# Performance work log

Hardware: AMD Instinct MI355X
Metric: run time of the kernel (lower is better)

The kernel has to match this reference:

```python
import jax, jax.numpy as jnp
import numpy as np

N_NODES = 50000
NODE_DIM = 128
HIDDEN = 128
N_EDGES = 1600000
N_POSTS = 8192


def setup_inputs() -> dict:
    key = jax.random.key(0)
    ks = jax.random.split(key, 12)
    glorot = lambda k, shp: jax.random.normal(k, shp, jnp.float32) * (1.0 / np.sqrt(shp[0]))
    inp = {
        "node_features": jax.random.normal(ks[0], (N_NODES, NODE_DIM), jnp.float32),
        "edge_index": jax.random.randint(ks[1], (2, N_EDGES), 0, N_NODES, jnp.int32),
        "post_mask": jax.random.randint(ks[2], (N_POSTS,), 0, N_NODES, jnp.int32),
        # node_encoder: node_dim -> hidden
        "W_enc": glorot(ks[3], (NODE_DIM, HIDDEN)),
        "b_enc": jnp.zeros((HIDDEN,), jnp.float32),
        # conv1/conv2: hidden -> hidden
        "W1": glorot(ks[4], (HIDDEN, HIDDEN)),
        "b1": jnp.zeros((HIDDEN,), jnp.float32),
        "W2": glorot(ks[5], (HIDDEN, HIDDEN)),
        "b2": jnp.zeros((HIDDEN,), jnp.float32),
        # output head: hidden -> hidden//2 -> 1
        "W_o1": glorot(ks[6], (HIDDEN, HIDDEN // 2)),
        "b_o1": jnp.zeros((HIDDEN // 2,), jnp.float32),
        "W_o2": glorot(ks[7], (HIDDEN // 2, 1)),
        "b_o2": jnp.zeros((1,), jnp.float32),
    }
    return inp


def _aggregate(h, src, dst, n_nodes):
    # sum_{e: dst[e]=v} h[src[e]]  -- vectorized scatter-add (segment_sum)
    return jax.ops.segment_sum(h[src], dst, num_segments=n_nodes)


def reference(node_features, edge_index, post_mask,
              W_enc, b_enc, W1, b1, W2, b2, W_o1, b_o1, W_o2, b_o2):
    src, dst = edge_index[0], edge_index[1]
    n = node_features.shape[0]

    h = jax.nn.relu(node_features @ W_enc + b_enc)          # [N, H]
    agg = _aggregate(h, src, dst, n)                        # [N, H]
    h = jax.nn.relu((agg + h) @ W1 + b1)
    agg = _aggregate(h, src, dst, n)
    h = jax.nn.relu((agg + h) @ W2 + b2)

    post = h[post_mask]                                     # [P, H]
    hid = jax.nn.relu(post @ W_o1 + b_o1)                   # [P, H//2]
    logits = (hid @ W_o2 + b_o2).squeeze(-1)                # [P]
    return jax.nn.sigmoid(logits)
```

## Files before the change

### kernel.cpp

```cpp
#include <hip/hip_runtime.h>
#include <math.h>


typedef unsigned long long u64;

#define RB_SIZE    4096
#define RB_ROUNDS  16
#define BUCKET_CAP 9216

__global__ __launch_bounds__(1024) void scan_part(const int* __restrict__ in,
                                                  int* __restrict__ bsum, int n) {
    __shared__ int red[1024];
    int i = blockIdx.x * 1024 + threadIdx.x;
    red[threadIdx.x] = (i < n) ? in[i] : 0;
    __syncthreads();
    for (int d = 512; d; d >>= 1) {
        if (threadIdx.x < d) red[threadIdx.x] += red[threadIdx.x + d];
        __syncthreads();
    }
    if (threadIdx.x == 0) bsum[blockIdx.x] = red[0];
}

__global__ __launch_bounds__(256) void scan_tops_par(const int* __restrict__ bsum,
                                                     int* __restrict__ bbase, int nb) {
    __shared__ int buf[256];
    int tid = threadIdx.x;
    int v = (tid < nb) ? bsum[tid] : 0;
    buf[tid] = v;
    __syncthreads();
    for (int s = 1; s < 256; s <<= 1) {
        int u = (tid >= s) ? buf[tid - s] : 0;
        __syncthreads();
        buf[tid] += u;
        __syncthreads();
    }
    if (tid < nb) bbase[tid] = buf[tid] - v;
}

__global__ __launch_bounds__(1024) void scan_final(const int* __restrict__ in,
                                                   const int* __restrict__ bbase,
                                                   int* __restrict__ out, int n) {
    __shared__ int buf[1024];
    int tid = threadIdx.x;
    int i = blockIdx.x * 1024 + tid;
    int c = (i < n) ? in[i] : 0;
    buf[tid] = c;
    __syncthreads();
    for (int d = 1; d < 1024; d <<= 1) {
        int v = (tid >= d) ? buf[tid - d] : 0;
        __syncthreads();
        buf[tid] += v;
        __syncthreads();
    }
    if (i < n) out[i] = bbase[blockIdx.x] + buf[tid] - c;
}

__global__ __launch_bounds__(256) void radix_hist_hi(const int* __restrict__ dstArr,
                                                     int* __restrict__ blockhist,
                                                     int E, int NBLK) {
    __shared__ int cnt[256];
    cnt[threadIdx.x] = 0;
    __syncthreads();
    int base = blockIdx.x * RB_SIZE;
    for (int t = threadIdx.x; t < RB_SIZE; t += 256) {
        int i = base + t;
        if (i < E) atomicAdd(&cnt[dstArr[i] >> 8], 1);
    }
    __syncthreads();
    blockhist[threadIdx.x * NBLK + blockIdx.x] = cnt[threadIdx.x];
}

__global__ __launch_bounds__(256) void radix_scatter_hi(const int* __restrict__ dstArr,
                                                        const int* __restrict__ srcArr,
                                                        u64* __restrict__ recOut,
                                                        const int* __restrict__ blockbase,
                                                        int E, int NBLK) {
    __shared__ int cursor[256];
    __shared__ int gbase[256];
    __shared__ int cnt[256 * 4];
    __shared__ int wbase[256 * 4];
    int tid = threadIdx.x;
    int wid = tid >> 6, lane = tid & 63;
    cursor[tid] = 0;
    gbase[tid] = blockbase[tid * NBLK + blockIdx.x];
    int base = blockIdx.x * RB_SIZE;
    __syncthreads();
    for (int r = 0; r < RB_ROUNDS; ++r) {
        int i = base + r * 256 + tid;
        bool valid = (i < E);
        int d = 0;
        u64 rec = 0;
        if (valid) {
            int dv = dstArr[i];
            rec = ((u64)(unsigned)srcArr[i] << 32) | (unsigned)dv;
            d = dv >> 8;
        }
        ((int4*)cnt)[tid] = make_int4(0, 0, 0, 0);
        u64 mask = ~0ull;
#pragma unroll
        for (int b = 0; b < 8; ++b) {
            int bit = (d >> b) & 1;
            u64 bal = __ballot(bit);
            mask &= bit ? bal : ~bal;
        }
        mask &= __ballot(valid ? 1 : 0);
        int rank = __popcll(mask & (((u64)1 << lane) - 1));
        int wtot = __popcll(mask);
        __syncthreads();
        if (valid && rank == 0) cnt[d * 4 + wid] = wtot;
        __syncthreads();
        {
            int run = cursor[tid];
#pragma unroll
            for (int w = 0; w < 4; ++w) {
                wbase[tid * 4 + w] = run;
                run += cnt[tid * 4 + w];
            }
            cursor[tid] = run;
        }
        __syncthreads();
        if (valid) recOut[gbase[d] + wbase[d * 4 + wid] + rank] = rec;
        __syncthreads();
    }
}

__global__ __launch_bounds__(256) void bucket_kernel(const u64* __restrict__ rec,
                                                     const int* __restrict__ blockbase,
                                                     int* __restrict__ csr_src,
                                                     int* __restrict__ offs,
                                                     int E, int N, int NBLK, int NDIG) {
    __shared__ int srcs[BUCKET_CAP];
    __shared__ unsigned char lob[BUCKET_CAP];
    __shared__ int binb[256];
    __shared__ int cursor[256];
    __shared__ int cnt4[256 * 4];
    __shared__ int wbase4[256 * 4];
    int g = blockIdx.x;
    int tid = threadIdx.x;
    int wid = tid >> 6, lane = tid & 63;
    int gbeg = blockbase[g * NBLK];
    int gend = (g + 1 < NDIG) ? blockbase[(g + 1) * NBLK] : E;
    int cnt = gend - gbeg;
    if (cnt > BUCKET_CAP) cnt = BUCKET_CAP;
    binb[tid] = 0;
    __syncthreads();
    for (int i = tid; i < cnt; i += 256) {
        u64 r = rec[gbeg + i];
        srcs[i] = (int)(r >> 32);
        int lo = (int)(r & 255);
        lob[i] = (unsigned char)lo;
        atomicAdd(&binb[lo], 1);
    }
    __syncthreads();
    int c = binb[tid];
    cursor[tid] = c;
    __syncthreads();
    for (int s = 1; s < 256; s <<= 1) {
        int v = (tid >= s) ? cursor[tid - s] : 0;
        __syncthreads();
        cursor[tid] += v;
        __syncthreads();
    }
    int excl = cursor[tid] - c;
    __syncthreads();
    binb[tid] = excl;
    cursor[tid] = excl;
    int v = g * 256 + tid;
    if (v < N) offs[v] = gbeg + excl;
    if (g == NDIG - 1 && tid == 0) offs[N] = E;
    __syncthreads();
    int nrounds = (cnt + 255) >> 8;
    for (int r = 0; r < nrounds; ++r) {
        int i = r * 256 + tid;
        bool valid = (i < cnt);
        int d = valid ? (int)lob[i] : 0;
        ((int4*)cnt4)[tid] = make_int4(0, 0, 0, 0);
        u64 mask = ~0ull;
#pragma unroll
        for (int b = 0; b < 8; ++b) {
            int bit = (d >> b) & 1;
            u64 bal = __ballot(bit);
            mask &= bit ? bal : ~bal;
        }
        mask &= __ballot(valid ? 1 : 0);
        int rank = __popcll(mask & (((u64)1 << lane) - 1));
        int wtot = __popcll(mask);
        __syncthreads();
        if (valid && rank == 0) cnt4[d * 4 + wid] = wtot;
        __syncthreads();
        {
            int run = cursor[tid];
#pragma unroll
            for (int w = 0; w < 4; ++w) {
                wbase4[tid * 4 + w] = run;
                run += cnt4[tid * 4 + w];
            }
            cursor[tid] = run;
        }
        __syncthreads();
        if (valid) csr_src[gbeg + wbase4[d * 4 + wid] + rank] = srcs[i];
        __syncthreads();
    }
}

template <bool FUSE>
__global__ __launch_bounds__(256) void gemm128(const float* __restrict__ A,
                                               const float* __restrict__ A2,
                                               const float* __restrict__ W,
                                               const float* __restrict__ bias,
                                               float* __restrict__ out, int M) {
    __shared__ float Ws[64 * 128];
    __shared__ float As[32 * 128];
    int tid = threadIdx.x;
    int row0 = blockIdx.x * 32;

    float4* As4 = (float4*)As;
#pragma unroll
    for (int i = 0; i < 4; ++i) {
        int idx = tid + 256 * i;
        int r = idx >> 5, c = idx & 31;
        int gr = row0 + r;
        float4 v = make_float4(0.f, 0.f, 0.f, 0.f);
        if (gr < M) {
            v = ((const float4*)A)[gr * 32 + c];
            if (FUSE) {
                float4 u = ((const float4*)A2)[gr * 32 + c];
                v.x += u.x; v.y += u.y; v.z += u.z; v.w += u.w;
            }
        }
        As4[idx] = v;
    }

    int tx = tid & 31, ty = tid >> 5;
    float acc[4][4];
#pragma unroll
    for (int r = 0; r < 4; ++r)
#pragma unroll
        for (int c = 0; c < 4; ++c) acc[r][c] = 0.f;

    const float4* W4 = (const float4*)W;
    float4* Ws4 = (float4*)Ws;

    for (int kh = 0; kh < 2; ++kh) {
        __syncthreads();
#pragma unroll
        for (int i = 0; i < 8; ++i)
            Ws4[tid + 256 * i] = W4[kh * 2048 + tid + 256 * i];
        __syncthreads();

#pragma unroll 2
        for (int k = 0; k < 64; k += 4) {
            float4 a[4], b[4];
#pragma unroll
            for (int r = 0; r < 4; ++r)
                a[r] = *(const float4*)&As[(ty * 4 + r) * 128 + kh * 64 + k];
#pragma unroll
            for (int kk = 0; kk < 4; ++kk)
                b[kk] = *(const float4*)&Ws[(k + kk) * 128 + tx * 4];
#pragma unroll
            for (int r = 0; r < 4; ++r) {
                acc[r][0] = fmaf(a[r].x, b[0].x, acc[r][0]);
                acc[r][1] = fmaf(a[r].x, b[0].y, acc[r][1]);
                acc[r][2] = fmaf(a[r].x, b[0].z, acc[r][2]);
                acc[r][3] = fmaf(a[r].x, b[0].w, acc[r][3]);
                acc[r][0] = fmaf(a[r].y, b[1].x, acc[r][0]);
                acc[r][1] = fmaf(a[r].y, b[1].y, acc[r][1]);
                acc[r][2] = fmaf(a[r].y, b[1].z, acc[r][2]);
                acc[r][3] = fmaf(a[r].y, b[1].w, acc[r][3]);
                acc[r][0] = fmaf(a[r].z, b[2].x, acc[r][0]);
                acc[r][1] = fmaf(a[r].z, b[2].y, acc[r][1]);
                acc[r][2] = fmaf(a[r].z, b[2].z, acc[r][2]);
                acc[r][3] = fmaf(a[r].z, b[2].w, acc[r][3]);
                acc[r][0] = fmaf(a[r].w, b[3].x, acc[r][0]);
                acc[r][1] = fmaf(a[r].w, b[3].y, acc[r][1]);
                acc[r][2] = fmaf(a[r].w, b[3].z, acc[r][2]);
                acc[r][3] = fmaf(a[r].w, b[3].w, acc[r][3]);
            }
        }
    }

    float4 bv = *(const float4*)&bias[tx * 4];
#pragma unroll
    for (int r = 0; r < 4; ++r) {
        int gr = row0 + ty * 4 + r;
        if (gr < M) {
            float4 o;
            o.x = fmaxf(acc[r][0] + bv.x, 0.f);
            o.y = fmaxf(acc[r][1] + bv.y, 0.f);
            o.z = fmaxf(acc[r][2] + bv.z, 0.f);
            o.w = fmaxf(acc[r][3] + bv.w, 0.f);
            ((float4*)out)[gr * 32 + tx] = o;
        }
    }
}

__global__ __launch_bounds__(256) void aggregate_kernel(const float* __restrict__ h,
                                                        const int* __restrict__ offs,
                                                        const int* __restrict__ csr_src,
                                                        float* __restrict__ agg, int n) {
    int w = (blockIdx.x * 256 + threadIdx.x) >> 6;
    int lane = threadIdx.x & 63;
    int half = lane >> 5;
    int l32 = lane & 31;
    int node = w * 2 + half;
    bool nvalid = node < n;
    int beg = 0, deg = 0;
    if (nvalid) {
        beg = offs[node];
        deg = offs[node + 1] - beg;
    }
    int mdeg = max(deg, __shfl_xor(deg, 32));
    const float4* h4 = (const float4*)h;
    float ax = 0.f, ay = 0.f, az = 0.f, aw = 0.f;
    for (int base = 0; base < mdeg; base += 32) {
        int idx = base + l32;
        int sv = (nvalid && idx < deg) ? csr_src[beg + idx] : 0;
        int nk = mdeg - base; if (nk > 32) nk = 32;
#pragma unroll 4
        for (int j = 0; j < nk; ++j) {
            int s = __shfl(sv, (half << 5) | j);
            if (base + j < deg) {
                float4 r = h4[s * 32 + l32];
                ax += r.x; ay += r.y; az += r.z; aw += r.w;
            }
        }
    }
    if (nvalid) {
        float4 o = make_float4(ax, ay, az, aw);
        ((float4*)agg)[(size_t)node * 32 + l32] = o;
    }
}

__global__ __launch_bounds__(256) void head_kernel(const float* __restrict__ h,
                                                   const int* __restrict__ mask,
                                                   const float* __restrict__ Wo1,
                                                   const float* __restrict__ bo1,
                                                   const float* __restrict__ Wo2,
                                                   const float* __restrict__ bo2,
                                                   float* __restrict__ out, int P) {
    __shared__ float hids[4][64];
    int wid = threadIdx.x >> 6;
    int lane = threadIdx.x & 63;
    int p = blockIdx.x * 4 + wid;
    if (p >= P) return;
    int node = mask[p];
    const float* row = h + (size_t)node * 128;
    float acc = 0.f;
#pragma unroll 4
    for (int k = 0; k < 128; ++k)
        acc = fmaf(row[k], Wo1[k * 64 + lane], acc);
    hids[wid][lane] = fmaxf(acc + bo1[lane], 0.f);
    if (lane == 0) {
        double lg = 0.0;
        for (int j = 0; j < 64; ++j)
            lg = fma((double)hids[wid][j], (double)Wo2[j], lg);
        lg += (double)bo2[0];
        out[p] = (float)(1.0 / (1.0 + exp(-lg)));
    }
}

extern "C" void kernel_launch(void* const* d_in, const int* in_sizes, int n_in,
                              void* d_out, int out_size, void* d_ws, size_t ws_size,
                              hipStream_t stream) {
    const float* NF   = (const float*)d_in[0];
    const int*   EI   = (const int*)d_in[1];
    const int*   MASK = (const int*)d_in[2];
    const float* Wenc = (const float*)d_in[3];
    const float* benc = (const float*)d_in[4];
    const float* W1   = (const float*)d_in[5];
    const float* b1   = (const float*)d_in[6];
    const float* W2   = (const float*)d_in[7];
    const float* b2   = (const float*)d_in[8];
    const float* Wo1  = (const float*)d_in[9];
    const float* bo1  = (const float*)d_in[10];
    const float* Wo2  = (const float*)d_in[11];
    const float* bo2  = (const float*)d_in[12];
    float* out = (float*)d_out;

    const int N = in_sizes[0] / 128;
    const int E = in_sizes[1] / 2;
    const int P = in_sizes[2];

    char* ws = (char*)d_ws;
    size_t off = 0;
    auto alloc = [&](size_t bytes) {
        char* pp = ws + off;
        off += (bytes + 255) & ~(size_t)255;
        return pp;
    };
    float* h       = (float*)alloc((size_t)N * 128 * 4);
    float* agg     = (float*)alloc((size_t)N * 128 * 4);
    int*   offs    = (int*)alloc((size_t)(N + 1) * 4);
    int*   csr_src = (int*)alloc((size_t)E * 4);
    const int NBLK = (E + RB_SIZE - 1) / RB_SIZE;
    int*   bh      = (int*)alloc((size_t)256 * NBLK * 4);
    int*   bb      = (int*)alloc((size_t)256 * NBLK * 4);
    int*   bsum    = (int*)alloc(256 * 4);
    int*   bbase   = (int*)alloc(256 * 4);
    u64* rec_a = (u64*)h;

    const int* src = EI;
    const int* dst = EI + E;

    const int NDIG = (N + 255) >> 8;
    const int L = NDIG * NBLK;
    const int nscanL = (L + 1023) / 1024;

    radix_hist_hi<<<NBLK, 256, 0, stream>>>(dst, bh, E, NBLK);
    scan_part<<<nscanL, 1024, 0, stream>>>(bh, bsum, L);
    scan_tops_par<<<1, 256, 0, stream>>>(bsum, bbase, nscanL);
    scan_final<<<nscanL, 1024, 0, stream>>>(bh, bbase, bb, L);
    radix_scatter_hi<<<NBLK, 256, 0, stream>>>(dst, src, rec_a, bb, E, NBLK);

    bucket_kernel<<<NDIG, 256, 0, stream>>>(rec_a, bb, csr_src, offs, E, N, NBLK, NDIG);

    int gblocks = (N + 31) / 32;
    int ablocks = ((N + 1) / 2 + 3) / 4;
    gemm128<false><<<gblocks, 256, 0, stream>>>(NF, nullptr, Wenc, benc, h, N);
    aggregate_kernel<<<ablocks, 256, 0, stream>>>(h, offs, csr_src, agg, N);
    gemm128<true><<<gblocks, 256, 0, stream>>>(h, agg, W1, b1, h, N);
    aggregate_kernel<<<ablocks, 256, 0, stream>>>(h, offs, csr_src, agg, N);
    gemm128<true><<<gblocks, 256, 0, stream>>>(h, agg, W2, b2, h, N);
    head_kernel<<<(P + 3) / 4, 256, 0, stream>>>(h, MASK, Wo1, bo1, Wo2, bo2, out, P);
}
```

Before: 397.3 us.

## Retile node GEMM to 128-row blocks with 8x8 register tiles and swizzled LDS

Each block of the dense 128x128 layer GEMM now covers 128 rows instead of 32, and each thread computes an 8x8 output tile instead of 4x4. The A tile is staged per K-half into shared memory with an XOR swizzle to avoid bank conflicts. The goal is more FMAs per shared-memory load and less redundant loading of W per row. In exchange the grid shrinks to about 391 blocks, each using 64 KB of LDS and more registers, which lowers occupancy and may leave CUs underfilled.

Result: no change. 395.6 us (median of 2 runs) (-0.4%).

```diff
diff --git a/kernel.cpp b/kernel.cpp
--- a/kernel.cpp
+++ b/kernel.cpp
@@ -209,87 +209,92 @@
                                                const float* __restrict__ W,
                                                const float* __restrict__ bias,
                                                float* __restrict__ out, int M) {
+    __shared__ float As[128 * 64];
     __shared__ float Ws[64 * 128];
-    __shared__ float As[32 * 128];
     int tid = threadIdx.x;
-    int row0 = blockIdx.x * 32;
-
+    int tx = tid & 15;
+    int ty = tid >> 4;
+    int row0 = blockIdx.x * 128;
+
+    float acc[8][8];
+#pragma unroll
+    for (int r = 0; r < 8; ++r)
+#pragma unroll
+        for (int c = 0; c < 8; ++c) acc[r][c] = 0.f;
+
+    const float4* A4 = (const float4*)A;
+    const float4* A24 = (const float4*)A2;
+    const float4* W4 = (const float4*)W;
     float4* As4 = (float4*)As;
-#pragma unroll
-    for (int i = 0; i < 4; ++i) {
-        int idx = tid + 256 * i;
-        int r = idx >> 5, c = idx & 31;
-        int gr = row0 + r;
-        float4 v = make_float4(0.f, 0.f, 0.f, 0.f);
+    float4* Ws4 = (float4*)Ws;
+    int swz = ty & 7;
+
+    for (int kh = 0; kh < 2; ++kh) {
+        __syncthreads();
+#pragma unroll
+        for (int j = 0; j < 8; ++j) {
+            int idx = tid + 256 * j;
+            int r = idx >> 4, kf = idx & 15;
+            int gr = row0 + r;
+            float4 v = make_float4(0.f, 0.f, 0.f, 0.f);
+            if (gr < M) {
+                v = A4[gr * 32 + kh * 16 + kf];
+                if (FUSE) {
+                    float4 u = A24[gr * 32 + kh * 16 + kf];
+                    v.x += u.x; v.y += u.y; v.z += u.z; v.w += u.w;
+                }
+            }
+            As4[r * 16 + (kf ^ ((r >> 3) & 7))] = v;
+            int k = idx >> 5, cf = idx & 31;
+            Ws4[k * 32 + cf] = W4[(kh * 64 + k) * 32 + cf];
+        }
+        __syncthreads();
+
+#pragma unroll 2
+        for (int k4 = 0; k4 < 16; ++k4) {
+            float4 a[8];
+#pragma unroll
+            for (int r = 0; r < 8; ++r)
+                a[r] = As4[(ty * 8 + r) * 16 + (k4 ^ swz)];
+#pragma unroll
+            for (int kk = 0; kk < 4; ++kk) {
+                float4 b0 = Ws4[(k4 * 4 + kk) * 32 + tx];
+                float4 b1 = Ws4[(k4 * 4 + kk) * 32 + 16 + tx];
+#pragma unroll
+                for (int r = 0; r < 8; ++r) {
+                    float av = (kk == 0) ? a[r].x : (kk == 1) ? a[r].y
+                             : (kk == 2) ? a[r].z : a[r].w;
+                    acc[r][0] = fmaf(av, b0.x, acc[r][0]);
+                    acc[r][1] = fmaf(av, b0.y, acc[r][1]);
+                    acc[r][2] = fmaf(av, b0.z, acc[r][2]);
+                    acc[r][3] = fmaf(av, b0.w, acc[r][3]);
+                    acc[r][4] = fmaf(av, b1.x, acc[r][4]);
+                    acc[r][5] = fmaf(av, b1.y, acc[r][5]);
+                    acc[r][6] = fmaf(av, b1.z, acc[r][6]);
+                    acc[r][7] = fmaf(av, b1.w, acc[r][7]);
+                }
+            }
+        }
+    }
+
+    float4 bv0 = ((const float4*)bias)[tx];
+    float4 bv1 = ((const float4*)bias)[16 + tx];
+    float4* out4 = (float4*)out;
+#pragma unroll
+    for (int r = 0; r < 8; ++r) {
+        int gr = row0 + ty * 8 + r;
         if (gr < M) {
-            v = ((const float4*)A)[gr * 32 + c];
-            if (FUSE) {
-                float4 u = ((const float4*)A2)[gr * 32 + c];
-                v.x += u.x; v.y += u.y; v.z += u.z; v.w += u.w;
-            }
-        }
-        As4[idx] = v;
-    }
-
-    int tx = tid & 31, ty = tid >> 5;
-    float acc[4][4];
-#pragma unroll
-    for (int r = 0; r < 4; ++r)
-#pragma unroll
-        for (int c = 0; c < 4; ++c) acc[r][c] = 0.f;
-
-    const float4* W4 = (const float4*)W;
-    float4* Ws4 = (float4*)Ws;
-
-    for (int kh = 0; kh < 2; ++kh) {
-        __syncthreads();
-#pragma unroll
-        for (int i = 0; i < 8; ++i)
-            Ws4[tid + 256 * i] = W4[kh * 2048 + tid + 256 * i];
-        __syncthreads();
-
-#pragma unroll 2
-        for (int k = 0; k < 64; k += 4) {
-            float4 a[4], b[4];
-#pragma unroll
-            for (int r = 0; r < 4; ++r)
-                a[r] = *(const float4*)&As[(ty * 4 + r) * 128 + kh * 64 + k];
-#pragma unroll
-            for (int kk = 0; kk < 4; ++kk)
-                b[kk] = *(const float4*)&Ws[(k + kk) * 128 + tx * 4];
-#pragma unroll
-            for (int r = 0; r < 4; ++r) {
-                acc[r][0] = fmaf(a[r].x, b[0].x, acc[r][0]);
-                acc[r][1] = fmaf(a[r].x, b[0].y, acc[r][1]);
-                acc[r][2] = fmaf(a[r].x, b[0].z, acc[r][2]);
-                acc[r][3] = fmaf(a[r].x, b[0].w, acc[r][3]);
-                acc[r][0] = fmaf(a[r].y, b[1].x, acc[r][0]);
-                acc[r][1] = fmaf(a[r].y, b[1].y, acc[r][1]);
-                acc[r][2] = fmaf(a[r].y, b[1].z, acc[r][2]);
-                acc[r][3] = fmaf(a[r].y, b[1].w, acc[r][3]);
-                acc[r][0] = fmaf(a[r].z, b[2].x, acc[r][0]);
-                acc[r][1] = fmaf(a[r].z, b[2].y, acc[r][1]);
-                acc[r][2] = fmaf(a[r].z, b[2].z, acc[r][2]);
-                acc[r][3] = fmaf(a[r].z, b[2].w, acc[r][3]);
-                acc[r][0] = fmaf(a[r].w, b[3].x, acc[r][0]);
-                acc[r][1] = fmaf(a[r].w, b[3].y, acc[r][1]);
-                acc[r][2] = fmaf(a[r].w, b[3].z, acc[r][2]);
-                acc[r][3] = fmaf(a[r].w, b[3].w, acc[r][3]);
-            }
-        }
-    }
-
-    float4 bv = *(const float4*)&bias[tx * 4];
-#pragma unroll
-    for (int r = 0; r < 4; ++r) {
-        int gr = row0 + ty * 4 + r;
-        if (gr < M) {
-            float4 o;
-            o.x = fmaxf(acc[r][0] + bv.x, 0.f);
-            o.y = fmaxf(acc[r][1] + bv.y, 0.f);
-            o.z = fmaxf(acc[r][2] + bv.z, 0.f);
-            o.w = fmaxf(acc[r][3] + bv.w, 0.f);
-            ((float4*)out)[gr * 32 + tx] = o;
+            float4 o0, o1;
+            o0.x = fmaxf(acc[r][0] + bv0.x, 0.f);
+            o0.y = fmaxf(acc[r][1] + bv0.y, 0.f);
+            o0.z = fmaxf(acc[r][2] + bv0.z, 0.f);
+            o0.w = fmaxf(acc[r][3] + bv0.w, 0.f);
+            o1.x = fmaxf(acc[r][4] + bv1.x, 0.f);
+            o1.y = fmaxf(acc[r][5] + bv1.y, 0.f);
+            o1.z = fmaxf(acc[r][6] + bv1.z, 0.f);
+            o1.w = fmaxf(acc[r][7] + bv1.w, 0.f);
+            out4[gr * 32 + tx] = o0;
+            out4[gr * 32 + 16 + tx] = o1;
         }
     }
 }
@@ -414,7 +419,7 @@
 
     bucket_kernel<<<NDIG, 256, 0, stream>>>(rec_a, bb, csr_src, offs, E, N, NBLK, NDIG);
 
-    int gblocks = (N + 31) / 32;
+    int gblocks = (N + 127) / 128;
     int ablocks = ((N + 1) / 2 + 3) / 4;
     gemm128<false><<<gblocks, 256, 0, stream>>>(NF, nullptr, Wenc, benc, h, N);
     aggregate_kernel<<<ablocks, 256, 0, stream>>>(h, offs, csr_src, agg, N);
```
